# Performance work log

Hardware: AMD Instinct MI355X
Metric: run time of the kernel (lower is better)

The kernel has to match this reference:

```python
import jax, jax.numpy as jnp
import numpy as np

EPS = 1e-8
TEMPERATURE = 1.0


def setup_inputs() -> dict:
    key = jax.random.key(0)
    basin_seq = jax.random.normal(key, (4, 512, 64), dtype=jnp.float32)
    residual_scale = jnp.ones((), dtype=jnp.float32)  # nn.Parameter(torch.tensor(1.0))
    return {"basin_seq": basin_seq, "residual_scale": residual_scale}


def _project_to_simplex(x):
    sp = jax.nn.softplus(x)
    p = sp / (sp.sum(axis=-1, keepdims=True) + EPS)
    return jnp.maximum(p, EPS)


def _qfi_attention_weights(x, temperature):
    # x: (B, T, D)
    p = _project_to_simplex(x)
    # fisher_rao_distance_simplex re-normalizes both operands
    p = p / (p.sum(axis=-1, keepdims=True) + EPS)
    # Faithful: eps is inside the sqrt, so this is a true (B,T,T,D) reduction,
    # not sqrt(p) @ sqrt(p)^T.
    inner = jnp.sqrt(p[:, :, None, :] * p[:, None, :, :] + EPS).sum(axis=-1)  # (B,T,T)
    inner = jnp.clip(inner, -1.0 + 1e-6, 1.0 - 1e-6)
    dist = 2.0 * jnp.arccos(inner)
    logits = -dist / max(float(temperature), 1e-6)
    return jax.nn.softmax(logits, axis=-1)  # (B,T,T)


def _phi_from_activations(acts):
    # acts: (B, T, D)
    t = acts.shape[1]
    x = acts - acts.mean(axis=1, keepdims=True)
    cov = jnp.einsum('btd,bte->bde', x, x) / (t + EPS)
    var = jnp.maximum(jnp.diagonal(cov, axis1=-2, axis2=-1), EPS)  # (B,D)
    denom = jnp.maximum(jnp.sqrt(var[:, :, None] * var[:, None, :]), EPS)
    corr = jnp.clip(cov / denom, -1.0, 1.0)
    d = corr.shape[-1]
    offdiag = corr * (1.0 - jnp.eye(d, dtype=corr.dtype))
    return jnp.abs(offdiag).mean(axis=(-2, -1))  # (B,)


def _kappa_proxy(x):
    return jnp.linalg.norm(x, axis=-1).mean(axis=-1)  # (B,)


def reference(basin_seq, residual_scale):
    x = basin_seq
    for _ in range(2):
        w = _qfi_attention_weights(x, TEMPERATURE)
        x_attn = jnp.einsum('bij,bjd->bid', w, x)
        x = 0.5 * x + 0.5 * x_attn
        x = x + 0.01 * residual_scale * (x_attn - x)
    phi = _phi_from_activations(x)
    kappa = _kappa_proxy(x)
    return (x, phi, kappa)
```

## Files before the change

kernel.cpp:

```cpp
#include <hip/hip_runtime.h>
#include <math.h>

#define B_ 4
#define T_ 512
#define D_ 64
#define EPS 1e-8f

__device__ __forceinline__ float wave_sum(float v) {
#pragma unroll
  for (int m = 1; m < 64; m <<= 1) v += __shfl_xor(v, m, 64);
  return v;
}
__device__ __forceinline__ float wave_max(float v) {
#pragma unroll
  for (int m = 1; m < 64; m <<= 1) v = fmaxf(v, __shfl_xor(v, m, 64));
  return v;
}
__device__ __forceinline__ float softplus_f(float x) {
  return fmaxf(x, 0.0f) + log1pf(expf(-fabsf(x)));
}

__global__ __launch_bounds__(256) void proj_kernel(const float* __restrict__ x,
                                                   float* __restrict__ s) {
  int wave = threadIdx.x >> 6, lane = threadIdx.x & 63;
  int row = blockIdx.x * 4 + wave;
  float sp = softplus_f(x[row * D_ + lane]);
  float s1 = wave_sum(sp);
  float p = sp / (s1 + EPS);
  p = fmaxf(p, EPS);
  float s2 = wave_sum(p);
  s[row * D_ + lane] = sqrtf(p / (s2 + EPS));
}

__global__ __launch_bounds__(256) void logits_kernel(const float* __restrict__ s,
                                                     float* __restrict__ L) {
  int jt = blockIdx.x, it = blockIdx.y, b = blockIdx.z;
  __shared__ float si[64][68];
  __shared__ float sj[64][68];
  int tid = threadIdx.x;
  const float* sb = s + b * T_ * D_;
#pragma unroll
  for (int k = 0; k < 4; ++k) {
    int idx = tid + k * 256;
    int row = idx >> 4, c4 = idx & 15;
    *(float4*)&si[row][c4 * 4] = *(const float4*)(sb + (it * 64 + row) * D_ + c4 * 4);
    *(float4*)&sj[row][c4 * 4] = *(const float4*)(sb + (jt * 64 + row) * D_ + c4 * 4);
  }
  __syncthreads();

  int i4 = tid >> 4, j4 = tid & 15;
  float acc[4][4];
#pragma unroll
  for (int a = 0; a < 4; ++a)
#pragma unroll
    for (int c = 0; c < 4; ++c) acc[a][c] = 0.f;

#pragma unroll 4
  for (int d4 = 0; d4 < 16; ++d4) {
    float4 A[4], Bv[4];
#pragma unroll
    for (int a = 0; a < 4; ++a) A[a] = *(const float4*)&si[i4 + 16 * a][d4 * 4];
#pragma unroll
    for (int c = 0; c < 4; ++c) Bv[c] = *(const float4*)&sj[j4 + 16 * c][d4 * 4];
#pragma unroll
    for (int a = 0; a < 4; ++a)
#pragma unroll
      for (int c = 0; c < 4; ++c) {
        acc[a][c] = fmaf(A[a].x, Bv[c].x, acc[a][c]);
        acc[a][c] = fmaf(A[a].y, Bv[c].y, acc[a][c]);
        acc[a][c] = fmaf(A[a].z, Bv[c].z, acc[a][c]);
        acc[a][c] = fmaf(A[a].w, Bv[c].w, acc[a][c]);
      }
  }
#pragma unroll
  for (int a = 0; a < 4; ++a) {
    int i = it * 64 + i4 + 16 * a;
    float* Lr = L + ((size_t)(b * T_) + i) * T_ + jt * 64;
#pragma unroll
    for (int c = 0; c < 4; ++c) {
      float inner = fminf(fmaxf(acc[a][c], -1.0f + 1e-6f), 1.0f - 1e-6f);
      Lr[j4 + 16 * c] = -2.0f * acosf(inner);
    }
  }
}

__global__ __launch_bounds__(256) void apply_kernel(const float* __restrict__ L,
                                                    const float* __restrict__ xin,
                                                    const float* __restrict__ rsp,
                                                    float* __restrict__ xout,
                                                    float* __restrict__ sout) {
  int b = blockIdx.y;
  int i0 = blockIdx.x * 8;
  __shared__ float wR[8][512];
  __shared__ float red[4][8][64];
  int tid = threadIdx.x;
  int w = tid >> 6, lane = tid & 63;

#pragma unroll
  for (int r = 0; r < 2; ++r) {
    int i = w * 2 + r;
    const float* Lr = L + ((size_t)(b * T_) + i0 + i) * T_;
    float4 v0 = ((const float4*)Lr)[lane];
    float4 v1 = ((const float4*)Lr)[64 + lane];
    float m = fmaxf(fmaxf(fmaxf(v0.x, v0.y), fmaxf(v0.z, v0.w)),
                    fmaxf(fmaxf(v1.x, v1.y), fmaxf(v1.z, v1.w)));
    m = wave_max(m);
    float4 e0, e1;
    e0.x = __expf(v0.x - m); e0.y = __expf(v0.y - m);
    e0.z = __expf(v0.z - m); e0.w = __expf(v0.w - m);
    e1.x = __expf(v1.x - m); e1.y = __expf(v1.y - m);
    e1.z = __expf(v1.z - m); e1.w = __expf(v1.w - m);
    float ssum = wave_sum(e0.x + e0.y + e0.z + e0.w + e1.x + e1.y + e1.z + e1.w);
    float inv = 1.0f / ssum;
    e0.x *= inv; e0.y *= inv; e0.z *= inv; e0.w *= inv;
    e1.x *= inv; e1.y *= inv; e1.z *= inv; e1.w *= inv;
    *(float4*)&wR[i][lane * 4] = e0;
    *(float4*)&wR[i][256 + lane * 4] = e1;
  }
  __syncthreads();

  int dg = tid & 15, js = tid >> 4;
  float acc[8][4];
#pragma unroll
  for (int i = 0; i < 8; ++i)
#pragma unroll
    for (int k = 0; k < 4; ++k) acc[i][k] = 0.f;

  const float* xb = xin + (size_t)(b * T_) * D_;
#pragma unroll 2
  for (int jj = 0; jj < 8; ++jj) {
    int jbase = jj * 64 + js * 4;
    float xr[4][4];
#pragma unroll
    for (int c = 0; c < 4; ++c) {
      float4 xv = *(const float4*)(xb + (jbase + c) * D_ + dg * 4);
      xr[c][0] = xv.x; xr[c][1] = xv.y; xr[c][2] = xv.z; xr[c][3] = xv.w;
    }
#pragma unroll
    for (int i = 0; i < 8; ++i) {
      float4 wv = *(const float4*)&wR[i][jbase];
      float wc[4] = {wv.x, wv.y, wv.z, wv.w};
#pragma unroll
      for (int c = 0; c < 4; ++c)
#pragma unroll
        for (int k = 0; k < 4; ++k)
          acc[i][k] = fmaf(wc[c], xr[c][k], acc[i][k]);
    }
  }

#pragma unroll
  for (int i = 0; i < 8; ++i)
#pragma unroll
    for (int k = 0; k < 4; ++k) {
      float v = acc[i][k];
      v += __shfl_xor(v, 16, 64);
      v += __shfl_xor(v, 32, 64);
      acc[i][k] = v;
    }
  if (lane < 16) {
#pragma unroll
    for (int i = 0; i < 8; ++i)
      *(float4*)&red[w][i][lane * 4] =
          make_float4(acc[i][0], acc[i][1], acc[i][2], acc[i][3]);
  }
  __syncthreads();

  float c01 = 0.01f * rsp[0];
#pragma unroll
  for (int h = 0; h < 2; ++h) {
    int i = w + 4 * h, d = lane;
    float xa = red[0][i][d] + red[1][i][d] + red[2][i][d] + red[3][i][d];
    size_t idx = ((size_t)(b * T_) + i0 + i) * D_ + d;
    float xn = 0.5f * (1.0f - c01) * xin[idx] + 0.5f * (1.0f + c01) * xa;
    xout[idx] = xn;
    float sp = softplus_f(xn);
    float s1 = wave_sum(sp);
    float p = sp / (s1 + EPS);
    p = fmaxf(p, EPS);
    float s2 = wave_sum(p);
    sout[idx] = sqrtf(p / (s2 + EPS));
  }
}

__global__ __launch_bounds__(256) void p1_kernel(const float* __restrict__ x,
                                                 float* __restrict__ covp,
                                                 float* __restrict__ meanp,
                                                 float* __restrict__ kappap) {
  int blk = blockIdx.x;
  int b = blk >> 3, sl = blk & 7;
  const float* xb = x + ((size_t)(b * T_) + sl * 64) * D_;
  __shared__ float tile[64][68];
  __shared__ float red2[4][64];
  __shared__ float kred[4];
  int tid = threadIdx.x;
#pragma unroll
  for (int k = 0; k < 4; ++k) {
    int idx = tid + k * 256;
    int row = idx >> 4, c4 = idx & 15;
    *(float4*)&tile[row][c4 * 4] = *(const float4*)(xb + row * D_ + c4 * 4);
  }
  __syncthreads();

  {
    int d = tid & 63, q = tid >> 6;
    float ms = 0.f;
#pragma unroll
    for (int tt = 0; tt < 16; ++tt) ms += tile[q * 16 + tt][d];
    red2[q][d] = ms;
  }

  {
    int tr = tid >> 2, qq = tid & 3;
    float ksq = 0.f;
#pragma unroll
    for (int k = 0; k < 16; ++k) {
      float v = tile[tr][qq * 16 + k];
      ksq = fmaf(v, v, ksq);
    }
    ksq += __shfl_xor(ksq, 1, 64);
    ksq += __shfl_xor(ksq, 2, 64);
    float contrib = (qq == 0) ? sqrtf(ksq) : 0.f;
    contrib = wave_sum(contrib);
    if ((tid & 63) == 0) kred[tid >> 6] = contrib;
  }

  int dd = tid >> 2, e16 = tid & 3;
  float acc[16];
#pragma unroll
  for (int k = 0; k < 16; ++k) acc[k] = 0.f;
  for (int tt = 0; tt < 64; ++tt) {
    float xd = tile[tt][dd];
    const float4* te = (const float4*)&tile[tt][e16 * 16];
    float4 v0 = te[0], v1 = te[1], v2 = te[2], v3 = te[3];
    acc[0]  = fmaf(xd, v0.x, acc[0]);  acc[1]  = fmaf(xd, v0.y, acc[1]);
    acc[2]  = fmaf(xd, v0.z, acc[2]);  acc[3]  = fmaf(xd, v0.w, acc[3]);
    acc[4]  = fmaf(xd, v1.x, acc[4]);  acc[5]  = fmaf(xd, v1.y, acc[5]);
    acc[6]  = fmaf(xd, v1.z, acc[6]);  acc[7]  = fmaf(xd, v1.w, acc[7]);
    acc[8]  = fmaf(xd, v2.x, acc[8]);  acc[9]  = fmaf(xd, v2.y, acc[9]);
    acc[10] = fmaf(xd, v2.z, acc[10]); acc[11] = fmaf(xd, v2.w, acc[11]);
    acc[12] = fmaf(xd, v3.x, acc[12]); acc[13] = fmaf(xd, v3.y, acc[13]);
    acc[14] = fmaf(xd, v3.z, acc[14]); acc[15] = fmaf(xd, v3.w, acc[15]);
  }
  float* cp = covp + (size_t)blk * 4096 + dd * 64 + e16 * 16;
#pragma unroll
  for (int kk = 0; kk < 4; ++kk)
    *(float4*)(cp + kk * 4) =
        make_float4(acc[kk * 4], acc[kk * 4 + 1], acc[kk * 4 + 2], acc[kk * 4 + 3]);
  __syncthreads();
  if (tid < 64)
    meanp[blk * 64 + tid] = red2[0][tid] + red2[1][tid] + red2[2][tid] + red2[3][tid];
  if (tid == 0) kappap[blk] = kred[0] + kred[1] + kred[2] + kred[3];
}

__global__ __launch_bounds__(256) void p2_kernel(const float* __restrict__ covp,
                                                 const float* __restrict__ meanp,
                                                 const float* __restrict__ kappap,
                                                 float* __restrict__ out) {
  int b = blockIdx.x;
  __shared__ float mu[64];
  __shared__ float var[64];
  __shared__ float phired[4];
  int tid = threadIdx.x;
  if (tid < 64) {
    float m = 0.f;
#pragma unroll
    for (int s = 0; s < 8; ++s) m += meanp[(b * 8 + s) * 64 + tid];
    mu[tid] = m * (1.0f / 512.0f);
  }
  __syncthreads();

  int dd = tid >> 2, e16 = tid & 3;
  float acc[16];
#pragma unroll
  for (int k = 0; k < 16; ++k) acc[k] = 0.f;
#pragma unroll
  for (int s = 0; s < 8; ++s) {
    const float* cp = covp + (size_t)(b * 8 + s) * 4096 + dd * 64 + e16 * 16;
#pragma unroll
    for (int kk = 0; kk < 4; ++kk) {
      float4 v = *(const float4*)(cp + kk * 4);
      acc[kk * 4] += v.x; acc[kk * 4 + 1] += v.y;
      acc[kk * 4 + 2] += v.z; acc[kk * 4 + 3] += v.w;
    }
  }
  float mud = mu[dd];
#pragma unroll
  for (int k = 0; k < 16; ++k)
    acc[k] = acc[k] * (1.0f / 512.0f) - mud * mu[e16 * 16 + k];
  if ((dd >> 4) == e16) var[dd] = fmaxf(acc[dd & 15], EPS);
  __syncthreads();

  float vd = var[dd];
  float psum = 0.f;
#pragma unroll
  for (int k = 0; k < 16; ++k) {
    int e = e16 * 16 + k;
    if (e == dd) continue;
    float denom = fmaxf(sqrtf(vd * var[e]), EPS);
    float cc = fminf(fmaxf(acc[k] / denom, -1.0f), 1.0f);
    psum += fabsf(cc);
  }
  psum = wave_sum(psum);
  if ((tid & 63) == 0) phired[tid >> 6] = psum;
  __syncthreads();
  if (tid == 0) {
    out[B_ * T_ * D_ + b] = (phired[0] + phired[1] + phired[2] + phired[3]) *
                            (1.0f / 4096.0f);
    float ks = 0.f;
#pragma unroll
    for (int s = 0; s < 8; ++s) ks += kappap[b * 8 + s];
    out[B_ * T_ * D_ + B_ + b] = ks * (1.0f / 512.0f);
  }
}

extern "C" void kernel_launch(void* const* d_in, const int* in_sizes, int n_in,
                              void* d_out, int out_size, void* d_ws, size_t ws_size,
                              hipStream_t stream) {
  const float* x0 = (const float*)d_in[0];
  const float* rs = (const float*)d_in[1];
  float* out = (float*)d_out;
  float* s     = (float*)d_ws;
  float* L     = s + B_ * T_ * D_;
  float* x1    = L + B_ * T_ * T_;
  float* covp  = x1 + B_ * T_ * D_;
  float* meanp = covp + 32 * 4096;
  float* kappap = meanp + 32 * 64;

  dim3 lgrd(8, 8, 4), agrd(64, 4);
  proj_kernel<<<(B_ * T_) / 4, 256, 0, stream>>>(x0, s);
  logits_kernel<<<lgrd, 256, 0, stream>>>(s, L);
  apply_kernel<<<agrd, 256, 0, stream>>>(L, x0, rs, x1, s);
  logits_kernel<<<lgrd, 256, 0, stream>>>(s, L);
  apply_kernel<<<agrd, 256, 0, stream>>>(L, x1, rs, out, s);
  p1_kernel<<<32, 256, 0, stream>>>(out, covp, meanp, kappap);
  p2_kernel<<<4, 256, 0, stream>>>(covp, meanp, kappap, out);
}
```

Before: 104.1 us.

## Fuse logits, softmax and weighted sum into one attention-iteration kernel

Replaces the separate logits and apply kernels with a single fiter kernel per iteration. Each block stages the whole batch's s vectors into 128KB of LDS using an XOR swizzle, computes an 8x512 logit strip, and runs softmax with cross-wave max and sum reductions. It then restages x into the same LDS buffer and performs the weighted sum, so the B×T×T logits matrix never goes to global memory. Ping-pong s buffers replace in-place reuse, and the phi/kappa reduction is split across 128 blocks with a 1024-thread final kernel. The cost is redundant per-block staging of the full 128KB batch and very low occupancy (one block per CU).

```diff
diff --git a/kernel.cpp b/kernel.cpp
--- a/kernel.cpp
+++ b/kernel.cpp
@@ -11,14 +11,12 @@
   for (int m = 1; m < 64; m <<= 1) v += __shfl_xor(v, m, 64);
   return v;
 }
-__device__ __forceinline__ float wave_max(float v) {
-#pragma unroll
-  for (int m = 1; m < 64; m <<= 1) v = fmaxf(v, __shfl_xor(v, m, 64));
-  return v;
-}
 __device__ __forceinline__ float softplus_f(float x) {
   return fmaxf(x, 0.0f) + log1pf(expf(-fabsf(x)));
 }
+
+#define DOT4(ACC, A, Bv) \
+  ACC = fmaf((A).x, (Bv).x, fmaf((A).y, (Bv).y, fmaf((A).z, (Bv).z, fmaf((A).w, (Bv).w, ACC))))
 
 __global__ __launch_bounds__(256) void proj_kernel(const float* __restrict__ x,
                                                    float* __restrict__ s) {
@@ -32,153 +30,185 @@
   s[row * D_ + lane] = sqrtf(p / (s2 + EPS));
 }
 
-__global__ __launch_bounds__(256) void logits_kernel(const float* __restrict__ s,
-                                                     float* __restrict__ L) {
-  int jt = blockIdx.x, it = blockIdx.y, b = blockIdx.z;
-  __shared__ float si[64][68];
-  __shared__ float sj[64][68];
-  int tid = threadIdx.x;
-  const float* sb = s + b * T_ * D_;
-#pragma unroll
-  for (int k = 0; k < 4; ++k) {
-    int idx = tid + k * 256;
-    int row = idx >> 4, c4 = idx & 15;
-    *(float4*)&si[row][c4 * 4] = *(const float4*)(sb + (it * 64 + row) * D_ + c4 * 4);
-    *(float4*)&sj[row][c4 * 4] = *(const float4*)(sb + (jt * 64 + row) * D_ + c4 * 4);
-  }
-  __syncthreads();
-
-  int i4 = tid >> 4, j4 = tid & 15;
-  float acc[4][4];
-#pragma unroll
-  for (int a = 0; a < 4; ++a)
-#pragma unroll
-    for (int c = 0; c < 4; ++c) acc[a][c] = 0.f;
-
-#pragma unroll 4
-  for (int d4 = 0; d4 < 16; ++d4) {
-    float4 A[4], Bv[4];
-#pragma unroll
-    for (int a = 0; a < 4; ++a) A[a] = *(const float4*)&si[i4 + 16 * a][d4 * 4];
-#pragma unroll
-    for (int c = 0; c < 4; ++c) Bv[c] = *(const float4*)&sj[j4 + 16 * c][d4 * 4];
-#pragma unroll
-    for (int a = 0; a < 4; ++a)
-#pragma unroll
-      for (int c = 0; c < 4; ++c) {
-        acc[a][c] = fmaf(A[a].x, Bv[c].x, acc[a][c]);
-        acc[a][c] = fmaf(A[a].y, Bv[c].y, acc[a][c]);
-        acc[a][c] = fmaf(A[a].z, Bv[c].z, acc[a][c]);
-        acc[a][c] = fmaf(A[a].w, Bv[c].w, acc[a][c]);
-      }
-  }
-#pragma unroll
-  for (int a = 0; a < 4; ++a) {
-    int i = it * 64 + i4 + 16 * a;
-    float* Lr = L + ((size_t)(b * T_) + i) * T_ + jt * 64;
-#pragma unroll
-    for (int c = 0; c < 4; ++c) {
-      float inner = fminf(fmaxf(acc[a][c], -1.0f + 1e-6f), 1.0f - 1e-6f);
-      Lr[j4 + 16 * c] = -2.0f * acosf(inner);
-    }
-  }
-}
-
-__global__ __launch_bounds__(256) void apply_kernel(const float* __restrict__ L,
-                                                    const float* __restrict__ xin,
+__device__ __forceinline__ void stage512(const float* __restrict__ g,
+                                         float* __restrict__ lds, int tid) {
+#pragma unroll
+  for (int h = 0; h < 2; ++h) {
+    float4 v[8];
+#pragma unroll
+    for (int r = 0; r < 8; ++r) {
+      int slot = (h * 8 + r) * 512 + tid;
+      int j = slot >> 4, c4 = slot & 15;
+      v[r] = *(const float4*)(g + j * 64 + ((c4 ^ ((j >> 2) & 7)) << 2));
+    }
+#pragma unroll
+    for (int r = 0; r < 8; ++r) {
+      int slot = (h * 8 + r) * 512 + tid;
+      int j = slot >> 4, c4 = slot & 15;
+      *(float4*)(lds + j * 64 + (c4 << 2)) = v[r];
+    }
+  }
+}
+
+__global__ __launch_bounds__(512) void fiter_kernel(const float* __restrict__ s_g,
+                                                    const float* __restrict__ x_g,
                                                     const float* __restrict__ rsp,
                                                     float* __restrict__ xout,
                                                     float* __restrict__ sout) {
-  int b = blockIdx.y;
-  int i0 = blockIdx.x * 8;
-  __shared__ float wR[8][512];
-  __shared__ float red[4][8][64];
+  int b = blockIdx.y, i0 = blockIdx.x * 8;
   int tid = threadIdx.x;
   int w = tid >> 6, lane = tid & 63;
-
-#pragma unroll
-  for (int r = 0; r < 2; ++r) {
-    int i = w * 2 + r;
-    const float* Lr = L + ((size_t)(b * T_) + i0 + i) * T_;
-    float4 v0 = ((const float4*)Lr)[lane];
-    float4 v1 = ((const float4*)Lr)[64 + lane];
-    float m = fmaxf(fmaxf(fmaxf(v0.x, v0.y), fmaxf(v0.z, v0.w)),
-                    fmaxf(fmaxf(v1.x, v1.y), fmaxf(v1.z, v1.w)));
-    m = wave_max(m);
-    float4 e0, e1;
-    e0.x = __expf(v0.x - m); e0.y = __expf(v0.y - m);
-    e0.z = __expf(v0.z - m); e0.w = __expf(v0.w - m);
-    e1.x = __expf(v1.x - m); e1.y = __expf(v1.y - m);
-    e1.z = __expf(v1.z - m); e1.w = __expf(v1.w - m);
-    float ssum = wave_sum(e0.x + e0.y + e0.z + e0.w + e1.x + e1.y + e1.z + e1.w);
-    float inv = 1.0f / ssum;
-    e0.x *= inv; e0.y *= inv; e0.z *= inv; e0.w *= inv;
-    e1.x *= inv; e1.y *= inv; e1.z *= inv; e1.w *= inv;
-    *(float4*)&wR[i][lane * 4] = e0;
-    *(float4*)&wR[i][256 + lane * 4] = e1;
-  }
-  __syncthreads();
-
-  int dg = tid & 15, js = tid >> 4;
-  float acc[8][4];
-#pragma unroll
-  for (int i = 0; i < 8; ++i)
-#pragma unroll
-    for (int k = 0; k < 4; ++k) acc[i][k] = 0.f;
-
-  const float* xb = xin + (size_t)(b * T_) * D_;
+  const float* sb = s_g + (size_t)b * (T_ * D_);
+  const float* xb = x_g + (size_t)b * (T_ * D_);
+
+  __shared__ __align__(16) float sx[512 * 64];
+  __shared__ __align__(16) float wlds[8 * 516];
+  __shared__ __align__(16) float redv[8 * 68];
+  __shared__ float redM[8][8];
+  __shared__ float redS[8][8];
+
+  stage512(sb, sx, tid);
+  __syncthreads();
+
+  int i4 = lane >> 4, j16 = lane & 15;
+  int ia0 = i0 + 2 * i4;
+  const float* A0 = sx + ia0 * 64;
+  const float* A1 = A0 + 64;
+  int mA0 = (ia0 >> 2) & 7, mA1 = ((ia0 + 1) >> 2) & 7;
+  const float* Bp = sx + (w * 64 + 4 * j16) * 64;
+  int mB = j16 & 7;
+
+  float acc[2][4];
+#pragma unroll
+  for (int r = 0; r < 2; ++r)
+#pragma unroll
+    for (int c = 0; c < 4; ++c) acc[r][c] = 0.f;
+
+#pragma unroll
+  for (int d4 = 0; d4 < 16; ++d4) {
+    float4 a0 = *(const float4*)(A0 + ((d4 ^ mA0) << 2));
+    float4 a1 = *(const float4*)(A1 + ((d4 ^ mA1) << 2));
+    int ob = (d4 ^ mB) << 2;
+    float4 b0 = *(const float4*)(Bp + ob);
+    float4 b1 = *(const float4*)(Bp + 64 + ob);
+    float4 b2 = *(const float4*)(Bp + 128 + ob);
+    float4 b3 = *(const float4*)(Bp + 192 + ob);
+    DOT4(acc[0][0], a0, b0); DOT4(acc[0][1], a0, b1);
+    DOT4(acc[0][2], a0, b2); DOT4(acc[0][3], a0, b3);
+    DOT4(acc[1][0], a1, b0); DOT4(acc[1][1], a1, b1);
+    DOT4(acc[1][2], a1, b2); DOT4(acc[1][3], a1, b3);
+  }
+
+  float S[2][4];
+#pragma unroll
+  for (int r = 0; r < 2; ++r)
+#pragma unroll
+    for (int c = 0; c < 4; ++c) {
+      float inner = fminf(fmaxf(acc[r][c], -1.0f + 1e-6f), 1.0f - 1e-6f);
+      S[r][c] = -2.0f * acosf(inner);
+    }
+
+  float m0 = fmaxf(fmaxf(S[0][0], S[0][1]), fmaxf(S[0][2], S[0][3]));
+  float m1 = fmaxf(fmaxf(S[1][0], S[1][1]), fmaxf(S[1][2], S[1][3]));
+#pragma unroll
+  for (int mm = 1; mm < 16; mm <<= 1) {
+    m0 = fmaxf(m0, __shfl_xor(m0, mm, 64));
+    m1 = fmaxf(m1, __shfl_xor(m1, mm, 64));
+  }
+  if (j16 == 0) { redM[2 * i4][w] = m0; redM[2 * i4 + 1][w] = m1; }
+  __syncthreads();
+
+  stage512(xb, sx, tid);
+
+  float M0 = redM[2 * i4][0], M1 = redM[2 * i4 + 1][0];
+#pragma unroll
+  for (int q = 1; q < 8; ++q) {
+    M0 = fmaxf(M0, redM[2 * i4][q]);
+    M1 = fmaxf(M1, redM[2 * i4 + 1][q]);
+  }
+  float e[2][4];
+  float sl0 = 0.f, sl1 = 0.f;
+#pragma unroll
+  for (int c = 0; c < 4; ++c) {
+    e[0][c] = __expf(S[0][c] - M0); sl0 += e[0][c];
+    e[1][c] = __expf(S[1][c] - M1); sl1 += e[1][c];
+  }
+#pragma unroll
+  for (int mm = 1; mm < 16; mm <<= 1) {
+    sl0 += __shfl_xor(sl0, mm, 64);
+    sl1 += __shfl_xor(sl1, mm, 64);
+  }
+  if (j16 == 0) { redS[2 * i4][w] = sl0; redS[2 * i4 + 1][w] = sl1; }
+  int wb = w * 64 + 4 * j16;
+#pragma unroll
+  for (int r = 0; r < 2; ++r)
+#pragma unroll
+    for (int c = 0; c < 4; ++c) wlds[(2 * i4 + r) * 516 + wb + c] = e[r][c];
+  __syncthreads();
+
+  int js = tid & 15, dg = (tid >> 4) & 15, ig = tid >> 8;
+  int xcol = ((dg ^ (js & 7)) << 2);
+  float pacc[4][4];
+#pragma unroll
+  for (int ii = 0; ii < 4; ++ii)
+#pragma unroll
+    for (int k = 0; k < 4; ++k) pacc[ii][k] = 0.f;
+
 #pragma unroll 2
   for (int jj = 0; jj < 8; ++jj) {
     int jbase = jj * 64 + js * 4;
-    float xr[4][4];
-#pragma unroll
-    for (int c = 0; c < 4; ++c) {
-      float4 xv = *(const float4*)(xb + (jbase + c) * D_ + dg * 4);
-      xr[c][0] = xv.x; xr[c][1] = xv.y; xr[c][2] = xv.z; xr[c][3] = xv.w;
-    }
-#pragma unroll
-    for (int i = 0; i < 8; ++i) {
-      float4 wv = *(const float4*)&wR[i][jbase];
-      float wc[4] = {wv.x, wv.y, wv.z, wv.w};
-#pragma unroll
-      for (int c = 0; c < 4; ++c)
-#pragma unroll
-        for (int k = 0; k < 4; ++k)
-          acc[i][k] = fmaf(wc[c], xr[c][k], acc[i][k]);
-    }
-  }
-
-#pragma unroll
-  for (int i = 0; i < 8; ++i)
+    const float* xr = sx + jbase * 64 + xcol;
+    float4 x0 = *(const float4*)(xr);
+    float4 x1 = *(const float4*)(xr + 64);
+    float4 x2 = *(const float4*)(xr + 128);
+    float4 x3 = *(const float4*)(xr + 192);
+#pragma unroll
+    for (int ii = 0; ii < 4; ++ii) {
+      float4 wv = *(const float4*)(wlds + (4 * ig + ii) * 516 + jbase);
+      pacc[ii][0] = fmaf(wv.x, x0.x, fmaf(wv.y, x1.x, fmaf(wv.z, x2.x, fmaf(wv.w, x3.x, pacc[ii][0]))));
+      pacc[ii][1] = fmaf(wv.x, x0.y, fmaf(wv.y, x1.y, fmaf(wv.z, x2.y, fmaf(wv.w, x3.y, pacc[ii][1]))));
+      pacc[ii][2] = fmaf(wv.x, x0.z, fmaf(wv.y, x1.z, fmaf(wv.z, x2.z, fmaf(wv.w, x3.z, pacc[ii][2]))));
+      pacc[ii][3] = fmaf(wv.x, x0.w, fmaf(wv.y, x1.w, fmaf(wv.z, x2.w, fmaf(wv.w, x3.w, pacc[ii][3]))));
+    }
+  }
+#pragma unroll
+  for (int ii = 0; ii < 4; ++ii)
 #pragma unroll
     for (int k = 0; k < 4; ++k) {
-      float v = acc[i][k];
-      v += __shfl_xor(v, 16, 64);
-      v += __shfl_xor(v, 32, 64);
-      acc[i][k] = v;
-    }
-  if (lane < 16) {
-#pragma unroll
-    for (int i = 0; i < 8; ++i)
-      *(float4*)&red[w][i][lane * 4] =
-          make_float4(acc[i][0], acc[i][1], acc[i][2], acc[i][3]);
-  }
-  __syncthreads();
-
-  float c01 = 0.01f * rsp[0];
-#pragma unroll
-  for (int h = 0; h < 2; ++h) {
-    int i = w + 4 * h, d = lane;
-    float xa = red[0][i][d] + red[1][i][d] + red[2][i][d] + red[3][i][d];
-    size_t idx = ((size_t)(b * T_) + i0 + i) * D_ + d;
-    float xn = 0.5f * (1.0f - c01) * xin[idx] + 0.5f * (1.0f + c01) * xa;
-    xout[idx] = xn;
+      float v = pacc[ii][k];
+      v += __shfl_xor(v, 1, 64);
+      v += __shfl_xor(v, 2, 64);
+      v += __shfl_xor(v, 4, 64);
+      v += __shfl_xor(v, 8, 64);
+      pacc[ii][k] = v;
+    }
+  if (js == 0) {
+#pragma unroll
+    for (int ii = 0; ii < 4; ++ii)
+      *(float4*)(redv + (4 * ig + ii) * 68 + (dg << 2)) =
+          make_float4(pacc[ii][0], pacc[ii][1], pacc[ii][2], pacc[ii][3]);
+  }
+  __syncthreads();
+
+  {
+    int row = w, d = lane;
+    float ssum = 0.f;
+#pragma unroll
+    for (int q = 0; q < 8; ++q) ssum += redS[row][q];
+    float xa = redv[row * 68 + d] / ssum;
+    int ir = i0 + row;
+    int mr = (ir >> 2) & 7;
+    float xv = sx[ir * 64 + (((d >> 2) ^ mr) << 2) + (d & 3)];
+    float c01 = 0.01f * rsp[0];
+    float xn = 0.5f * (1.0f - c01) * xv + 0.5f * (1.0f + c01) * xa;
+    size_t gi = ((size_t)(b * T_) + ir) * D_ + d;
+    xout[gi] = xn;
     float sp = softplus_f(xn);
     float s1 = wave_sum(sp);
     float p = sp / (s1 + EPS);
     p = fmaxf(p, EPS);
     float s2 = wave_sum(p);
-    sout[idx] = sqrtf(p / (s2 + EPS));
+    sout[gi] = sqrtf(p / (s2 + EPS));
   }
 }
 
@@ -187,48 +217,49 @@
                                                  float* __restrict__ meanp,
                                                  float* __restrict__ kappap) {
   int blk = blockIdx.x;
-  int b = blk >> 3, sl = blk & 7;
-  const float* xb = x + ((size_t)(b * T_) + sl * 64) * D_;
-  __shared__ float tile[64][68];
+  int b = blk >> 5, sl = blk & 31;
+  const float* xb = x + ((size_t)(b * T_) + sl * 16) * D_;
+  __shared__ float tile[16][68];
   __shared__ float red2[4][64];
   __shared__ float kred[4];
   int tid = threadIdx.x;
-#pragma unroll
-  for (int k = 0; k < 4; ++k) {
-    int idx = tid + k * 256;
-    int row = idx >> 4, c4 = idx & 15;
+  {
+    int row = tid >> 4, c4 = tid & 15;
     *(float4*)&tile[row][c4 * 4] = *(const float4*)(xb + row * D_ + c4 * 4);
   }
   __syncthreads();
+
+  {
+    int tr = tid >> 4, qq = tid & 15;
+    float ksq = 0.f;
+#pragma unroll
+    for (int k = 0; k < 4; ++k) {
+      float v = tile[tr][qq * 4 + k];
+      ksq = fmaf(v, v, ksq);
+    }
+    ksq += __shfl_xor(ksq, 1, 64);
+    ksq += __shfl_xor(ksq, 2, 64);
+    ksq += __shfl_xor(ksq, 4, 64);
+    ksq += __shfl_xor(ksq, 8, 64);
+    float contrib = (qq == 0) ? sqrtf(ksq) : 0.f;
+    contrib = wave_sum(contrib);
+    if ((tid & 63) == 0) kred[tid >> 6] = contrib;
+  }
 
   {
     int d = tid & 63, q = tid >> 6;
     float ms = 0.f;
 #pragma unroll
-    for (int tt = 0; tt < 16; ++tt) ms += tile[q * 16 + tt][d];
+    for (int tt = 0; tt < 4; ++tt) ms += tile[q * 4 + tt][d];
     red2[q][d] = ms;
-  }
-
-  {
-    int tr = tid >> 2, qq = tid & 3;
-    float ksq = 0.f;
-#pragma unroll
-    for (int k = 0; k < 16; ++k) {
-      float v = tile[tr][qq * 16 + k];
-      ksq = fmaf(v, v, ksq);
-    }
-    ksq += __shfl_xor(ksq, 1, 64);
-    ksq += __shfl_xor(ksq, 2, 64);
-    float contrib = (qq == 0) ? sqrtf(ksq) : 0.f;
-    contrib = wave_sum(contrib);
-    if ((tid & 63) == 0) kred[tid >> 6] = contrib;
   }
 
   int dd = tid >> 2, e16 = tid & 3;
   float acc[16];
 #pragma unroll
   for (int k = 0; k < 16; ++k) acc[k] = 0.f;
-  for (int tt = 0; tt < 64; ++tt) {
+#pragma unroll
+  for (int tt = 0; tt < 16; ++tt) {
     float xd = tile[tt][dd];
     const float4* te = (const float4*)&tile[tt][e16 * 16];
     float4 v0 = te[0], v1 = te[1], v2 = te[2], v3 = te[3];
@@ -252,49 +283,42 @@
   if (tid == 0) kappap[blk] = kred[0] + kred[1] + kred[2] + kred[3];
 }
 
-__global__ __launch_bounds__(256) void p2_kernel(const float* __restrict__ covp,
-                                                 const float* __restrict__ meanp,
-                                                 const float* __restrict__ kappap,
-                                                 float* __restrict__ out) {
+__global__ __launch_bounds__(1024) void p2_kernel(const float* __restrict__ covp,
+                                                  const float* __restrict__ meanp,
+                                                  const float* __restrict__ kappap,
+                                                  float* __restrict__ out) {
   int b = blockIdx.x;
   __shared__ float mu[64];
   __shared__ float var[64];
-  __shared__ float phired[4];
+  __shared__ float phired[16];
   int tid = threadIdx.x;
   if (tid < 64) {
     float m = 0.f;
 #pragma unroll
-    for (int s = 0; s < 8; ++s) m += meanp[(b * 8 + s) * 64 + tid];
+    for (int s = 0; s < 32; ++s) m += meanp[(b * 32 + s) * 64 + tid];
     mu[tid] = m * (1.0f / 512.0f);
   }
   __syncthreads();
 
-  int dd = tid >> 2, e16 = tid & 3;
-  float acc[16];
-#pragma unroll
-  for (int k = 0; k < 16; ++k) acc[k] = 0.f;
-#pragma unroll
-  for (int s = 0; s < 8; ++s) {
-    const float* cp = covp + (size_t)(b * 8 + s) * 4096 + dd * 64 + e16 * 16;
-#pragma unroll
-    for (int kk = 0; kk < 4; ++kk) {
-      float4 v = *(const float4*)(cp + kk * 4);
-      acc[kk * 4] += v.x; acc[kk * 4 + 1] += v.y;
-      acc[kk * 4 + 2] += v.z; acc[kk * 4 + 3] += v.w;
-    }
+  int dd = tid >> 4, e4 = tid & 15;
+  float acc[4] = {0.f, 0.f, 0.f, 0.f};
+#pragma unroll
+  for (int s = 0; s < 32; ++s) {
+    float4 v = *(const float4*)(covp + (size_t)(b * 32 + s) * 4096 + dd * 64 + e4 * 4);
+    acc[0] += v.x; acc[1] += v.y; acc[2] += v.z; acc[3] += v.w;
   }
   float mud = mu[dd];
 #pragma unroll
-  for (int k = 0; k < 16; ++k)
-    acc[k] = acc[k] * (1.0f / 512.0f) - mud * mu[e16 * 16 + k];
-  if ((dd >> 4) == e16) var[dd] = fmaxf(acc[dd & 15], EPS);
+  for (int k = 0; k < 4; ++k)
+    acc[k] = acc[k] * (1.0f / 512.0f) - mud * mu[e4 * 4 + k];
+  if (e4 == (dd >> 2)) var[dd] = fmaxf(acc[dd & 3], EPS);
   __syncthreads();
 
   float vd = var[dd];
   float psum = 0.f;
 #pragma unroll
-  for (int k = 0; k < 16; ++k) {
-    int e = e16 * 16 + k;
+  for (int k = 0; k < 4; ++k) {
+    int e = e4 * 4 + k;
     if (e == dd) continue;
     float denom = fmaxf(sqrtf(vd * var[e]), EPS);
     float cc = fminf(fmaxf(acc[k] / denom, -1.0f), 1.0f);
@@ -304,11 +328,13 @@
   if ((tid & 63) == 0) phired[tid >> 6] = psum;
   __syncthreads();
   if (tid == 0) {
-    out[B_ * T_ * D_ + b] = (phired[0] + phired[1] + phired[2] + phired[3]) *
-                            (1.0f / 4096.0f);
+    float ph = 0.f;
+#pragma unroll
+    for (int q = 0; q < 16; ++q) ph += phired[q];
+    out[B_ * T_ * D_ + b] = ph * (1.0f / 4096.0f);
     float ks = 0.f;
 #pragma unroll
-    for (int s = 0; s < 8; ++s) ks += kappap[b * 8 + s];
+    for (int s = 0; s < 32; ++s) ks += kappap[b * 32 + s];
     out[B_ * T_ * D_ + B_ + b] = ks * (1.0f / 512.0f);
   }
 }
@@ -319,19 +345,17 @@
   const float* x0 = (const float*)d_in[0];
   const float* rs = (const float*)d_in[1];
   float* out = (float*)d_out;
-  float* s     = (float*)d_ws;
-  float* L     = s + B_ * T_ * D_;
-  float* x1    = L + B_ * T_ * T_;
+  float* s0    = (float*)d_ws;
+  float* s1    = s0 + B_ * T_ * D_;
+  float* x1    = s1 + B_ * T_ * D_;
   float* covp  = x1 + B_ * T_ * D_;
-  float* meanp = covp + 32 * 4096;
-  float* kappap = meanp + 32 * 64;
-
-  dim3 lgrd(8, 8, 4), agrd(64, 4);
-  proj_kernel<<<(B_ * T_) / 4, 256, 0, stream>>>(x0, s);
-  logits_kernel<<<lgrd, 256, 0, stream>>>(s, L);
-  apply_kernel<<<agrd, 256, 0, stream>>>(L, x0, rs, x1, s);
-  logits_kernel<<<lgrd, 256, 0, stream>>>(s, L);
-  apply_kernel<<<agrd, 256, 0, stream>>>(L, x1, rs, out, s);
-  p1_kernel<<<32, 256, 0, stream>>>(out, covp, meanp, kappap);
-  p2_kernel<<<4, 256, 0, stream>>>(covp, meanp, kappap, out);
-}
+  float* meanp = covp + 128 * 4096;
+  float* kappap = meanp + 128 * 64;
+
+  dim3 fgrd(64, 4);
+  proj_kernel<<<(B_ * T_) / 4, 256, 0, stream>>>(x0, s0);
+  fiter_kernel<<<fgrd, 512, 0, stream>>>(s0, x0, rs, x1, s1);
+  fiter_kernel<<<fgrd, 512, 0, stream>>>(s1, x1, rs, out, s0);
+  p1_kernel<<<128, 256, 0, stream>>>(out, covp, meanp, kappap);
+  p2_kernel<<<4, 1024, 0, stream>>>(covp, meanp, kappap, out);
+}
```

Measured after the change: 96.12 us. 1.08x faster.
